# Kernel tuning notes

Hardware: AMD Instinct MI355X
Metric: run time of the kernel (lower is better)

Reference implementation:

```python
import jax, jax.numpy as jnp
import numpy as np

B, N, H, R = 128, 512, 256, 3
VIRTUAL_DECAY = 0.7


def _build_tree():
    # Deterministic random recursive tree: parent[i] ~ U[0, i)
    rng = np.random.default_rng(0)
    parent = np.zeros(N, np.int64)
    for i in range(1, N):
        parent[i] = rng.integers(0, i)
    depth = np.zeros(N, np.int64)
    for i in range(1, N):
        depth[i] = depth[parent[i]] + 1
    rel_edge = rng.integers(0, R, N)          # relation type of edge (parent -> i)
    virtual = rng.random(N) < 0.1
    children = [[] for _ in range(N)]
    for i in range(1, N):
        children[parent[i]].append(i)
    # Group internal nodes by depth (deepest first == valid post-order batching),
    # pad ragged child lists per level.
    levels = []
    for d in range(int(depth.max()), -1, -1):
        nodes = [n for n in range(N) if depth[n] == d and len(children[n]) > 0]
        if not nodes:
            continue
        cmax = max(len(children[n]) for n in nodes)
        M = len(nodes)
        cidx = np.zeros((M, cmax), np.int64)
        cmask = np.zeros((M, cmax), np.float32)
        crel = np.zeros((M, cmax), np.int64)
        cvirt = np.zeros((M, cmax), bool)
        for m, n in enumerate(nodes):
            ch = children[n]
            k = len(ch)
            cidx[m, :k] = ch
            cmask[m, :k] = 1.0
            crel[m, :k] = rel_edge[ch]
            cvirt[m, :k] = virtual[ch]
        levels.append((jnp.array(nodes), jnp.array(cidx), jnp.array(cmask),
                       jnp.array(crel), jnp.array(cvirt)))
    return levels

LEVELS = _build_tree()


def _forward(node_features, W_enc, b_enc, rel_emb, W_i, b_i, W_o, b_o, W_u, b_u,
             W_f, b_f, w_attn, b_attn):
    h = node_features @ W_enc + b_enc            # (B, N, H) node_encoder
    c = jnp.zeros_like(h)
    for node_ids, cidx, cmask, crel, cvirt in LEVELS:
        x = h[:, node_ids]                       # (B, M, H) input_vec (== encoded feats)
        ch_h = h[:, cidx]                        # (B, M, C, H)
        ch_c = c[:, cidx]
        # virtual-node decay + padding mask
        decay = jnp.where(cvirt, VIRTUAL_DECAY, 1.0).astype(h.dtype) * cmask  # (M, C)
        ch_h = ch_h * decay[None, :, :, None]
        ch_c = ch_c * decay[None, :, :, None]
        # relation-aware attention over children
        re = rel_emb[crel]                       # (M, C, H)
        scores = jnp.einsum('bmch,h->bmc', re[None] + ch_h, w_attn) + b_attn[0]
        scores = jnp.where(cmask[None] > 0, scores, -1e9)
        attw = jax.nn.softmax(scores, axis=-1)   # (B, M, C)
        h_sum = jnp.einsum('bmc,bmch->bmh', attw, ch_h)
        # per-relation forget transform (note: original applies NO sigmoid here)
        f = jnp.zeros_like(ch_h)
        for r in range(R):
            fr = jnp.einsum('bmch,hk->bmck', ch_h, W_f[r]) + b_f[r]
            f = f + fr * (crel == r).astype(h.dtype)[None, :, :, None]
        c_sum = jnp.sum(f * ch_c, axis=2)        # (B, M, H); padded ch_c is 0
        comb = jnp.concatenate([x, h_sum], axis=-1)  # (B, M, 2H)
        i_g = jax.nn.sigmoid(comb @ W_i + b_i)
        o_g = jax.nn.sigmoid(comb @ W_o + b_o)
        u_g = jnp.tanh(comb @ W_u + b_u)
        c_new = i_g * u_g + c_sum
        h_new = o_g * jnp.tanh(c_new)
        h = h.at[:, node_ids].set(h_new)
        c = c.at[:, node_ids].set(c_new)
    return h[:, 0]                               # pooling == 'root' (root = 0)


def setup_inputs() -> dict:
    key = jax.random.key(0)
    ks = jax.random.split(key, 8)
    s = 0.05
    f32 = jnp.float32
    return {
        'node_features': jax.random.normal(ks[0], (B, N, H), f32),
        'W_enc': jax.random.normal(ks[1], (H, H), f32) * s,
        'b_enc': jnp.full((H,), 0.1, f32),
        'rel_emb': jax.random.normal(ks[2], (R, H), f32) * s,
        'W_i': jax.random.normal(ks[3], (2 * H, H), f32) * s,
        'b_i': jnp.full((H,), 0.1, f32),
        'W_o': jax.random.normal(ks[4], (2 * H, H), f32) * s,
        'b_o': jnp.full((H,), 0.1, f32),
        'W_u': jax.random.normal(ks[5], (2 * H, H), f32) * s,
        'b_u': jnp.full((H,), 0.1, f32),
        'W_f': jax.random.normal(ks[6], (R, H, H), f32) * s,
        'b_f': jnp.full((R, H), 0.1, f32),
        'w_attn': jax.random.normal(ks[7], (H,), f32) * s,
        'b_attn': jnp.full((1,), 0.1, f32),
    }


def reference(node_features, W_enc, b_enc, rel_emb, W_i, b_i, W_o, b_o, W_u, b_u,
              W_f, b_f, w_attn, b_attn):
    return _forward(node_features, W_enc, b_enc, rel_emb, W_i, b_i, W_o, b_o,
                    W_u, b_u, W_f, b_f, w_attn, b_attn)
```

## Files before the change

### kernel.cpp

```cpp
#include <hip/hip_runtime.h>
#include <stdint.h>
#include <string.h>
#include <math.h>

#define NB 128
#define NN 512
#define NH 256
#define NR 3
#define TH_SPLIT 16

typedef __attribute__((ext_vector_type(8))) short bh8;
typedef __attribute__((ext_vector_type(4))) float f32x4;

struct Pcg {
  __uint128_t state, inc;
  bool has32; uint32_t buf32;
};

static const __uint128_t PCG_MULT =
    (((__uint128_t)2549297995355413924ULL) << 64) | 4865540595714422341ULL;

static inline uint64_t pcg_next64(Pcg& s) {
  s.state = s.state * PCG_MULT + s.inc;
  uint64_t hi = (uint64_t)(s.state >> 64), lo = (uint64_t)s.state;
  uint64_t x = hi ^ lo;
  unsigned rot = (unsigned)(s.state >> 122) & 63u;
  return (x >> rot) | (x << ((64u - rot) & 63u));
}
static inline uint32_t pcg_next32(Pcg& s) {
  if (s.has32) { s.has32 = false; return s.buf32; }
  uint64_t n = pcg_next64(s);
  s.has32 = true; s.buf32 = (uint32_t)(n >> 32);
  return (uint32_t)n;
}
static inline uint64_t pcg_bounded(Pcg& s, uint64_t high) {
  uint64_t rng = high - 1;
  if (rng == 0) return 0;
  uint32_t rng_excl = (uint32_t)rng + 1u;
  uint64_t m = (uint64_t)pcg_next32(s) * (uint64_t)rng_excl;
  uint32_t leftover = (uint32_t)m;
  if (leftover < rng_excl) {
    uint32_t threshold = (uint32_t)((0xFFFFFFFFu - (uint32_t)rng) % rng_excl);
// ... 19 lines not shown
  };
  for (int i = 0; i < 4; i++) pool[i] = hashmix(0u);
  for (int src = 0; src < 4; src++)
    for (int dst = 0; dst < 4; dst++)
      if (src != dst) pool[dst] = mix(pool[dst], hashmix(pool[src]));
  uint32_t gs[8]; uint32_t hb = 0x8b51f9ddu;
  for (int i = 0; i < 8; i++) {
    uint32_t dv = pool[i & 3];
    dv ^= hb; hb *= 0x58f38dedu; dv *= hb; dv ^= dv >> 16;
    gs[i] = dv;
  }
  uint64_t w0 = (uint64_t)gs[0] | ((uint64_t)gs[1] << 32);
  uint64_t w1 = (uint64_t)gs[2] | ((uint64_t)gs[3] << 32);
  uint64_t w2 = (uint64_t)gs[4] | ((uint64_t)gs[5] << 32);
  uint64_t w3 = (uint64_t)gs[6] | ((uint64_t)gs[7] << 32);
  __uint128_t initstate = (((__uint128_t)w0) << 64) | w1;
  __uint128_t initseq   = (((__uint128_t)w2) << 64) | w3;
  s.state = 0;
  s.inc = (initseq << 1) | 1;
  s.state = s.state * PCG_MULT + s.inc;
  s.state += initstate;
  s.state = s.state * PCG_MULT + s.inc;
  s.has32 = false; s.buf32 = 0;
}

struct TreeMeta {
  int nodes[512];
  int cstart[512];
  int ccount[512];
  int echild[512];
  int erel[512];
  float edecay[512];
  int cechild[512];
  int cerel[512];
  float cedec[512];
  int cens[513];
};
struct HostTree {
  TreeMeta meta;
  int n_levels;
  int level_off[520];
  int level_M[520];
};

static void build_tree_host(HostTree& T) {
  Pcg st; pcg_seed0(st);
  int parent[NN], depth[NN], rel[NN];
  unsigned char virt[NN];
  parent[0] = 0; depth[0] = 0;
  for (int i = 1; i < NN; i++) parent[i] = (int)pcg_bounded(st, (uint64_t)i);
  for (int i = 1; i < NN; i++) depth[i] = depth[parent[i]] + 1;
  for (int i = 0; i < NN; i++) rel[i] = (int)pcg_bounded(st, (uint64_t)NR);
  for (int i = 0; i < NN; i++) virt[i] = (pcg_double(st) < 0.1) ? 1 : 0;

  int childcnt[NN]; memset(childcnt, 0, sizeof(childcnt));
  for (int i = 1; i < NN; i++) childcnt[parent[i]]++;
  int maxd = 0;
  for (int i = 0; i < NN; i++) if (depth[i] > maxd) maxd = depth[i];

  int ni = 0, ne = 0, nec = 0;
  T.n_levels = 0;
  for (int d = maxd; d >= 0; d--) {
    int mstart = ni;
    for (int n = 0; n < NN; n++) {
      if (depth[n] == d && childcnt[n] > 0) {
        T.meta.nodes[ni] = n;
        T.meta.cstart[ni] = ne;
        T.meta.ccount[ni] = childcnt[n];
        T.meta.cens[ni] = nec;
        for (int i2 = 1; i2 < NN; i2++) {
          if (parent[i2] == n) {
            T.meta.echild[ne] = i2;
            T.meta.erel[ne] = rel[i2];
            T.meta.edecay[ne] = virt[i2] ? 0.7f : 1.0f;
            ne++;
            if (childcnt[i2] > 0) {
              T.meta.cechild[nec] = i2;
              T.meta.cerel[nec] = rel[i2];
              T.meta.cedec[nec] = virt[i2] ? 0.7f : 1.0f;
              nec++;
            }
          }
        }
        ni++;
      }
    }
    if (ni > mstart) {
      T.level_off[T.n_levels] = mstart;
      T.level_M[T.n_levels] = ni - mstart;
      T.n_levels++;
    }
  }
  T.meta.cens[ni] = nec;
}

__device__ __forceinline__ uint16_t f2bf(float f) {
  uint32_t u = __float_as_uint(f);
  return (uint16_t)((u + 0x7fffu + ((u >> 16) & 1u)) >> 16);
}
__device__ __forceinline__ float bf2f(uint16_t b) {
  return __uint_as_float(((uint32_t)b) << 16);
}
__device__ __forceinline__ float sigm(float x) {
  return 1.f / (1.f + expf(-x));
}

__device__ __forceinline__ void stage_bf16(uint16_t* __restrict__ sm,
    const uint16_t* __restrict__ src, int stride, int rows) {
  const int chunks = rows << 3;
  for (int cch = threadIdx.x; cch < chunks; cch += 256) {
// ... 84 lines not shown
  }
#pragma unroll
  for (int i = 0; i < 4; i++) {
#pragma unroll
    for (int j = 0; j < 4; j++) {
      const int col = bn + wc2 * 64 + j * 16 + (lane & 15);
      const float be = b_enc[col];
#pragma unroll
      for (int r = 0; r < 4; r++) {
        const int row = bm + wr * 64 + i * 16 + (lane >> 4) * 4 + r;
        const uint16_t hv = f2bf(acc[i][j][r] + be);
        h_bf[(size_t)row * NH + col] = hv;
        x_enc[(size_t)row * NH + col] = hv;
      }
    }
  }
}

__global__ __launch_bounds__(256) void k_sv0(const uint16_t* __restrict__ h_bf,
    const float* __restrict__ w_attn, float* __restrict__ svp) {
  const int idx = blockIdx.x * 256 + threadIdx.x;
  const int g = idx & 15;
  const size_t row = (size_t)(idx >> 4);
  const uint16_t* hp = h_bf + row * NH + g * 16;
  uint4 p0 = *(const uint4*)hp, p1 = *(const uint4*)(hp + 8);
  const uint16_t* e0 = (const uint16_t*)&p0;
  const uint16_t* e1 = (const uint16_t*)&p1;
  float s = 0.f;
#pragma unroll
  for (int u = 0; u < 8; u++) s = fmaf(bf2f(e0[u]), w_attn[g * 16 + u], s);
#pragma unroll
  for (int u = 0; u < 8; u++) s = fmaf(bf2f(e1[u]), w_attn[g * 16 + 8 + u], s);
  svp[idx] = s;
}

__global__ __launch_bounds__(256) void k_att(
    const uint16_t* __restrict__ h_bf, const float* __restrict__ svp,
    const float* __restrict__ rel_emb, const float* __restrict__ w_attn,
    const float* __restrict__ b_attn, uint16_t* __restrict__ comb,
    const TreeMeta* __restrict__ tm, int nb) {
  __shared__ float sc[64 * 65];
  __shared__ float sRE[3];
  __shared__ int chl[64]; __shared__ int rll[64]; __shared__ float dcl[64];
  const int mloc = blockIdx.x >> 1, b0 = (blockIdx.x & 1) * 64;
  const int gi = nb + mloc;
  const int cs = tm->cstart[gi], cc = tm->ccount[gi];
  const int tid = threadIdx.x, wid = tid >> 6, lane = tid & 63;

  if (tid < cc) {
    chl[tid] = tm->echild[cs + tid];
    rll[tid] = tm->erel[cs + tid];
    dcl[tid] = tm->edecay[cs + tid];
  }
  if (wid < 3) {
    float p = 0.f;
#pragma unroll
    for (int i = 0; i < 4; i++) p += rel_emb[wid * NH + lane + 64 * i] * w_attn[lane + 64 * i];
#pragma unroll
    for (int off = 32; off; off >>= 1) p += __shfl_down(p, off);
    if (lane == 0) sRE[wid] = p;
  }
  __syncthreads();

  const float ba = b_attn[0];
  if (tid < 64) {
    const float* svpb = svp + (size_t)(b0 + tid) * NN * 16;
    for (int e = 0; e < cc; e++) {
      const float4* p = (const float4*)(svpb + chl[e] * 16);
      float4 a = p[0], b2 = p[1], c2 = p[2], d2 = p[3];
      float s = ((a.x + a.y) + (a.z + a.w)) + ((b2.x + b2.y) + (b2.z + b2.w)) +
                ((c2.x + c2.y) + (c2.z + c2.w)) + ((d2.x + d2.y) + (d2.z + d2.w));
      sc[tid * 65 + e] = sRE[rll[e]] + dcl[e] * s + ba;
    }
    float mx = -1e30f;
    for (int e = 0; e < cc; e++) mx = fmaxf(mx, sc[tid * 65 + e]);
    float ss = 0.f;
    for (int e = 0; e < cc; e++) ss += expf(sc[tid * 65 + e] - mx);
    const float inv = 1.0f / ss;
    for (int e = 0; e < cc; e++) sc[tid * 65 + e] = expf(sc[tid * 65 + e] - mx) * inv * dcl[e];
  }
  __syncthreads();

  const int sb = tid >> 2, sq = tid & 3;
  float hs[64];
#pragma unroll
  for (int v = 0; v < 64; v++) hs[v] = 0.f;
  const uint16_t* hbase = h_bf + (size_t)(b0 + sb) * NN * NH + sq * 64;
  uint4 bufA[8], bufB[8];
  LDROW(bufA, chl[0]);
  int e = 0;
  for (; e + 2 <= cc; e += 2) {
    LDROW(bufB, chl[e + 1]);
    ACCROW(bufA, sc[sb * 65 + e]);
    if (e + 2 < cc) LDROW(bufA, chl[e + 2]);
    ACCROW(bufB, sc[sb * 65 + e + 1]);
  }
  if (e < cc) ACCROW(bufA, sc[sb * 65 + e]);
  uint16_t* cb = comb + ((size_t)(mloc * 128 + b0 + sb)) * 256 + sq * 64;
#pragma unroll
  for (int v = 0; v < 8; v++) {
    uint4 w;
    w.x = (uint32_t)f2bf(hs[8 * v + 0]) | ((uint32_t)f2bf(hs[8 * v + 1]) << 16);
    w.y = (uint32_t)f2bf(hs[8 * v + 2]) | ((uint32_t)f2bf(hs[8 * v + 3]) << 16);
    w.z = (uint32_t)f2bf(hs[8 * v + 4]) | ((uint32_t)f2bf(hs[8 * v + 5]) << 16);
    w.w = (uint32_t)f2bf(hs[8 * v + 6]) | ((uint32_t)f2bf(hs[8 * v + 7]) << 16);
    *(uint4*)(cb + v * 8) = w;
  }
}

__global__ __launch_bounds__(256) void k_gat(
    uint16_t* h_bf, float* c, float* __restrict__ svp,
    const uint16_t* __restrict__ x_enc, const uint16_t* __restrict__ comb,
    const uint16_t* __restrict__ WfT, const uint16_t* __restrict__ WgT,
    const float* __restrict__ b_f, const float* __restrict__ b_i,
    const float* __restrict__ b_o, const float* __restrict__ b_u,
    const float* __restrict__ w_attn, float* __restrict__ out,
    const TreeMeta* __restrict__ tm, int nb) {
  const int bx = blockIdx.x, mloc = bx >> 1, b0 = (bx & 1) * 64;
  const int cslice = blockIdx.y * 64;
  const int gi = nb + mloc;
  const int nd = tm->nodes[gi];
  const int ce0 = tm->cens[gi], nic = tm->cens[gi + 1] - ce0;
  const int tid = threadIdx.x, wid = tid >> 6, lane = tid & 63;
  const int lr2 = lane & 15, hi4 = (lane >> 4), lk = hi4 << 3;
  const int colw = cslice + wid * 16 + lr2;

  f32x4 csum[4] = {};
#pragma unroll 2
  for (int e = 0; e < nic; e++) {
    const int ch = tm->cechild[ce0 + e];
    const int rel = tm->cerel[ce0 + e];
    const float dec = tm->cedec[ce0 + e];
    const uint16_t* Wr = WfT + (size_t)rel * 65536 + (size_t)colw * 256;
    f32x4 facc[4] = {};
#pragma unroll
    for (int k0 = 0; k0 < 8; k0++) {
      const int kk = k0 * 32 + lk;
      bh8 af[4];
#pragma unroll
      for (int i = 0; i < 4; i++)
        af[i] = *(const bh8*)(h_bf + ((size_t)(b0 + i * 16 + lr2) * NN + ch) * NH + kk);
      const bh8 bq = *(const bh8*)(Wr + kk);
#pragma unroll
      for (int i = 0; i < 4; i++)
        facc[i] = __builtin_amdgcn_mfma_f32_16x16x32_bf16(af[i], bq, facc[i], 0, 0, 0);
    }
    const float bfv = b_f[rel * NH + colw];
#pragma unroll
    for (int i = 0; i < 4; i++) {
#pragma unroll
      for (int r = 0; r < 4; r++) {
        const int brow = b0 + i * 16 + hi4 * 4 + r;
        const float cch = c[((size_t)brow * NN + ch) * NH + colw];
        csum[i][r] += (dec * facc[i][r] + bfv) * (dec * cch);
      }
    }
  }

  f32x4 ga[3][4] = {};
#pragma unroll
  for (int k32 = 0; k32 < 16; k32++) {
    const int kk = k32 * 32 + lk;
    bh8 af[4], bq[3];
    if (k32 < 8) {
#pragma unroll
      for (int i = 0; i < 4; i++)
        af[i] = *(const bh8*)(x_enc + ((size_t)(b0 + i * 16 + lr2) * NN + nd) * NH + kk);
    } else {
#pragma unroll
      for (int i = 0; i < 4; i++)
        af[i] = *(const bh8*)(comb + ((size_t)(mloc * 128 + b0 + i * 16 + lr2)) * 256 + (kk - 256));
    }
#pragma unroll
    for (int g = 0; g < 3; g++)
      bq[g] = *(const bh8*)(WgT + ((size_t)g << 17) + (size_t)colw * 512 + kk);
#pragma unroll
    for (int g = 0; g < 3; g++)
#pragma unroll
      for (int i = 0; i < 4; i++)
        ga[g][i] = __builtin_amdgcn_mfma_f32_16x16x32_bf16(af[i], bq[g], ga[g][i], 0, 0, 0);
  }

  const float bi_ = b_i[colw], bo_ = b_o[colw], bu_ = b_u[colw];
  const float wac = w_attn[colw];
#pragma unroll
  for (int i = 0; i < 4; i++) {
#pragma unroll
    for (int r = 0; r < 4; r++) {
      const int brow = b0 + i * 16 + hi4 * 4 + r;
      const size_t idx = ((size_t)brow * NN + nd) * NH + colw;
      const float ig = sigm(ga[0][i][r] + bi_);
      const float og = sigm(ga[1][i][r] + bo_);
      const float ug = tanhf(ga[2][i][r] + bu_);
      const float cn = fmaf(ig, ug, csum[i][r]);
      c[idx] = cn;
      const float hn = og * tanhf(cn);
      h_bf[idx] = f2bf(hn);
      if (nd == 0) out[(size_t)brow * NH + colw] = hn;
      float pv = hn * wac;
      pv += __shfl_xor(pv, 1); pv += __shfl_xor(pv, 2);
      pv += __shfl_xor(pv, 4); pv += __shfl_xor(pv, 8);
      if (lr2 == 0) svp[((size_t)brow * NN + nd) * 16 + (cslice >> 4) + wid] = pv;
    }
  }
}

__global__ __launch_bounds__(256) void k_tiny(
    uint16_t* h_bf, float* c, float* __restrict__ svp,
    const uint16_t* __restrict__ x_enc,
    const uint16_t* __restrict__ WfT, const uint16_t* __restrict__ WgT,
    const float* __restrict__ b_f, const float* __restrict__ b_i,
    const float* __restrict__ b_o, const float* __restrict__ b_u,
    const float* __restrict__ rel_emb, const float* __restrict__ w_attn,
    const float* __restrict__ b_attn, float* __restrict__ out,
    const TreeMeta* __restrict__ tm, int nb) {
  __shared__ float sc[64 * 65];
  __shared__ float swa[256];
  __shared__ float sRE[3];
  __shared__ int chl[64]; __shared__ int rll[64]; __shared__ float dcl[64];
  __shared__ __align__(16) uint16_t hsum[4 * 4096];

  const int c0 = blockIdx.x * 16;
  const int mloc = blockIdx.y >> 1, b0 = (blockIdx.y & 1) * 64;
  const int gi = nb + mloc;
  const int nd = tm->nodes[gi], cs = tm->cstart[gi], cc = tm->ccount[gi];
  const int ce0 = tm->cens[gi], nic = tm->cens[gi + 1] - ce0;
  const int tid = threadIdx.x, wid = tid >> 6, lane = tid & 63;
  const int lb = lane & 15, lq = lane >> 4;
  const int colw = c0 + lb;
  const int wrow = b0 + wid * 16;

  if (tid < cc) {
    chl[tid] = tm->echild[cs + tid];
    rll[tid] = tm->erel[cs + tid];
    dcl[tid] = tm->edecay[cs + tid];
  }
  swa[tid] = w_attn[tid];
// ... 82 lines not shown
    const int kk = k32 * 32 + lq * 8;
    bh8 af;
    if (k32 < 8) {
      af = *(const bh8*)(x_enc + ((size_t)(wrow + lb) * NN + nd) * NH + kk);
    } else {
      const int kx = k32 - 8;
      af = fld(hsum + (kx >> 1) * 4096, wid * 16 + lb, (kx & 1) * 32 + lq * 8);
    }
#pragma unroll
    for (int g = 0; g < 3; g++) {
      const bh8 bq = *(const bh8*)(WgT + ((size_t)g << 17) + (size_t)colw * 512 + kk);
      ga[g] = __builtin_amdgcn_mfma_f32_16x16x32_bf16(af, bq, ga[g], 0, 0, 0);
    }
  }

  const float bi_ = b_i[colw], bo_ = b_o[colw], bu_ = b_u[colw];
  const float wac = swa[colw];
#pragma unroll
  for (int r = 0; r < 4; r++) {
    const int brow = wrow + lq * 4 + r;
    const size_t idx = ((size_t)brow * NN + nd) * NH + colw;
    const float ig = sigm(ga[0][r] + bi_);
    const float og = sigm(ga[1][r] + bo_);
    const float ug = tanhf(ga[2][r] + bu_);
    const float cn = fmaf(ig, ug, csum[r]);
    c[idx] = cn;
    const float hn = og * tanhf(cn);
    h_bf[idx] = f2bf(hn);
    if (nd == 0) out[(size_t)brow * NH + colw] = hn;
    float pv = hn * wac;
    pv += __shfl_xor(pv, 1); pv += __shfl_xor(pv, 2);
    pv += __shfl_xor(pv, 4); pv += __shfl_xor(pv, 8);
    if (lb == 0) svp[((size_t)brow * NN + nd) * 16 + (c0 >> 4)] = pv;
  }
}

extern "C" void kernel_launch(void* const* d_in, const int* in_sizes, int n_in,
                              void* d_out, int out_size, void* d_ws, size_t ws_size,
                              hipStream_t stream) {
  (void)in_sizes; (void)n_in; (void)out_size; (void)ws_size;
  const float* nf      = (const float*)d_in[0];
  const float* W_enc   = (const float*)d_in[1];
  const float* b_enc   = (const float*)d_in[2];
  const float* rel_emb = (const float*)d_in[3];
  const float* W_i     = (const float*)d_in[4];
  const float* b_i     = (const float*)d_in[5];
  const float* W_o     = (const float*)d_in[6];
  const float* b_o     = (const float*)d_in[7];
  const float* W_u     = (const float*)d_in[8];
  const float* b_u     = (const float*)d_in[9];
  const float* W_f     = (const float*)d_in[10];
  const float* b_f     = (const float*)d_in[11];
  const float* w_attn  = (const float*)d_in[12];
  const float* b_attn  = (const float*)d_in[13];
  float* out = (float*)d_out;

  static HostTree T;
  build_tree_host(T);

  char* ws = (char*)d_ws;
  const size_t OFF_HBF  = 32768;
  const size_t SZ_HBF   = (size_t)NB * NN * NH * 2;
  const size_t OFF_XE   = OFF_HBF + SZ_HBF;
  const size_t OFF_WET  = OFF_XE + SZ_HBF;
  const size_t OFF_WFT  = OFF_WET + 131072;
  const size_t OFF_WGT  = OFF_WFT + 393216;
  const size_t OFF_C    = OFF_WGT + 786432;
  const size_t SZ_C     = (size_t)NB * NN * NH * 4;
  const size_t OFF_SVP  = OFF_C + SZ_C;
  const size_t OFF_COMB = OFF_SVP + (size_t)NB * NN * 16 * 4;

  TreeMeta* dm = (TreeMeta*)ws;
  uint16_t* h_bf = (uint16_t*)(ws + OFF_HBF);
  uint16_t* x_enc = (uint16_t*)(ws + OFF_XE);
  uint16_t* WeT = (uint16_t*)(ws + OFF_WET);
  uint16_t* WfT = (uint16_t*)(ws + OFF_WFT);
  uint16_t* WgT = (uint16_t*)(ws + OFF_WGT);
  float* c = (float*)(ws + OFF_C);
  float* svp = (float*)(ws + OFF_SVP);
  uint16_t* comb = (uint16_t*)(ws + OFF_COMB);

  hipMemcpyAsync(dm, &T.meta, sizeof(TreeMeta), hipMemcpyHostToDevice, stream);

  k_prep<<<2560, 256, 0, stream>>>(W_enc, W_f, W_i, W_o, W_u, WeT, WfT, WgT);
  k_enc<<<dim3((NB * NN) / 128, 2), 256, 0, stream>>>(nf, WeT, b_enc, h_bf, x_enc);
  k_sv0<<<dim3((NB * NN * 16) / 256), 256, 0, stream>>>(h_bf, w_attn, svp);

  for (int l = 0; l < T.n_levels; l++) {
    const int Mfull = T.level_M[l];
    if (Mfull >= TH_SPLIT) {
      for (int c0 = 0; c0 < Mfull; c0 += 128) {
        const int Mc = (Mfull - c0) < 128 ? (Mfull - c0) : 128;
        const int nb = T.level_off[l] + c0;
        k_att<<<dim3(2 * Mc), 256, 0, stream>>>(h_bf, svp, rel_emb, w_attn,
            b_attn, comb, dm, nb);
        k_gat<<<dim3(2 * Mc, 4), 256, 0, stream>>>(h_bf, c, svp, x_enc, comb,
            WfT, WgT, b_f, b_i, b_o, b_u, w_attn, out, dm, nb);
      }
    } else {
      k_tiny<<<dim3(16, 2 * Mfull), 256, 0, stream>>>(h_bf, c, svp, x_enc,
          WfT, WgT, b_f, b_i, b_o, b_u, rel_emb, w_attn, b_attn, out, dm,
          T.level_off[l]);
    }
  }
}
```

Before: 703.6 us.

## Fuse attention into level kernel and split high-fanout nodes with atomic forget-gate blocks

Replaces the per-level k_att+k_gat pair with a fused k_lvl that computes the attention-weighted child sum into shared memory (swizzled bf16) and feeds it straight into the gate MFMAs, removing the comb round trip and one launch per level. For levels containing a node with many internal children, the forget-gate child GEMMs are spread over extra blocks in a combined k_ac kernel that accumulates f*c into the parent cell state via atomicAdd, followed by a separate k_gates kernel. The tiny-level threshold changes and c is now zeroed with a memset so atomics accumulate correctly. Fusing lowers launch and global-traffic cost but uses a large shared-memory footprint per block, and the atomic path makes float summation order nondeterministic.

New measurement: 622.7 us. -11.5%, faster.

```diff
diff --git a/kernel.cpp b/kernel.cpp
--- a/kernel.cpp
+++ b/kernel.cpp
@@ -7,7 +7,8 @@
 #define NN 512
 #define NH 256
 #define NR 3
-#define TH_SPLIT 16
+#define TH_TINY 24
+#define SPLIT_NIC 16
 
 typedef __attribute__((ext_vector_type(8))) short bh8;
 typedef __attribute__((ext_vector_type(4))) float f32x4;
@@ -93,6 +94,7 @@
   int erel[512];
   float edecay[512];
   int cechild[512];
+  int cepar[512];
   int cerel[512];
   float cedec[512];
   int cens[513];
@@ -137,6 +139,7 @@
             ne++;
             if (childcnt[i2] > 0) {
               T.meta.cechild[nec] = i2;
+              T.meta.cepar[nec] = n;
               T.meta.cerel[nec] = rel[i2];
               T.meta.cedec[nec] = virt[i2] ? 0.7f : 1.0f;
               nec++;
@@ -289,24 +292,36 @@
   svp[idx] = s;
 }
 
-__global__ __launch_bounds__(256) void k_att(
-    const uint16_t* __restrict__ h_bf, const float* __restrict__ svp,
+__global__ __launch_bounds__(256) void k_lvl(
+    uint16_t* h_bf, float* c, float* __restrict__ svp,
+    const uint16_t* __restrict__ x_enc,
+    const uint16_t* __restrict__ WfT, const uint16_t* __restrict__ WgT,
+    const float* __restrict__ b_f, const float* __restrict__ b_i,
+    const float* __restrict__ b_o, const float* __restrict__ b_u,
     const float* __restrict__ rel_emb, const float* __restrict__ w_attn,
-    const float* __restrict__ b_attn, uint16_t* __restrict__ comb,
+    const float* __restrict__ b_attn, float* __restrict__ out,
     const TreeMeta* __restrict__ tm, int nb) {
   __shared__ float sc[64 * 65];
+  __shared__ float swa[256];
   __shared__ float sRE[3];
   __shared__ int chl[64]; __shared__ int rll[64]; __shared__ float dcl[64];
-  const int mloc = blockIdx.x >> 1, b0 = (blockIdx.x & 1) * 64;
+  __shared__ __align__(16) uint16_t hsum[4 * 4096];
+
+  const int bx = blockIdx.x, mloc = bx >> 1, b0 = (bx & 1) * 64;
+  const int cslice = blockIdx.y * 64;
   const int gi = nb + mloc;
-  const int cs = tm->cstart[gi], cc = tm->ccount[gi];
+  const int nd = tm->nodes[gi], cs = tm->cstart[gi], cc = tm->ccount[gi];
+  const int ce0 = tm->cens[gi], nic = tm->cens[gi + 1] - ce0;
   const int tid = threadIdx.x, wid = tid >> 6, lane = tid & 63;
+  const int lr2 = lane & 15, hi4 = (lane >> 4), lk = hi4 << 3;
+  const int colw = cslice + wid * 16 + lr2;
 
   if (tid < cc) {
     chl[tid] = tm->echild[cs + tid];
     rll[tid] = tm->erel[cs + tid];
     dcl[tid] = tm->edecay[cs + tid];
   }
+  swa[tid] = w_attn[tid];
   if (wid < 3) {
     float p = 0.f;
 #pragma unroll
@@ -337,48 +352,29 @@
   __syncthreads();
 
   const int sb = tid >> 2, sq = tid & 3;
-  float hs[64];
-#pragma unroll
-  for (int v = 0; v < 64; v++) hs[v] = 0.f;
-  const uint16_t* hbase = h_bf + (size_t)(b0 + sb) * NN * NH + sq * 64;
-  uint4 bufA[8], bufB[8];
-  LDROW(bufA, chl[0]);
-  int e = 0;
-  for (; e + 2 <= cc; e += 2) {
-    LDROW(bufB, chl[e + 1]);
-    ACCROW(bufA, sc[sb * 65 + e]);
-    if (e + 2 < cc) LDROW(bufA, chl[e + 2]);
-    ACCROW(bufB, sc[sb * 65 + e + 1]);
-  }
-  if (e < cc) ACCROW(bufA, sc[sb * 65 + e]);
-  uint16_t* cb = comb + ((size_t)(mloc * 128 + b0 + sb)) * 256 + sq * 64;
-#pragma unroll
-  for (int v = 0; v < 8; v++) {
-    uint4 w;
-    w.x = (uint32_t)f2bf(hs[8 * v + 0]) | ((uint32_t)f2bf(hs[8 * v + 1]) << 16);
-    w.y = (uint32_t)f2bf(hs[8 * v + 2]) | ((uint32_t)f2bf(hs[8 * v + 3]) << 16);
-    w.z = (uint32_t)f2bf(hs[8 * v + 4]) | ((uint32_t)f2bf(hs[8 * v + 5]) << 16);
-    w.w = (uint32_t)f2bf(hs[8 * v + 6]) | ((uint32_t)f2bf(hs[8 * v + 7]) << 16);
-    *(uint4*)(cb + v * 8) = w;
-  }
-}
-
-__global__ __launch_bounds__(256) void k_gat(
-    uint16_t* h_bf, float* c, float* __restrict__ svp,
-    const uint16_t* __restrict__ x_enc, const uint16_t* __restrict__ comb,
-    const uint16_t* __restrict__ WfT, const uint16_t* __restrict__ WgT,
-    const float* __restrict__ b_f, const float* __restrict__ b_i,
-    const float* __restrict__ b_o, const float* __restrict__ b_u,
-    const float* __restrict__ w_attn, float* __restrict__ out,
-    const TreeMeta* __restrict__ tm, int nb) {
-  const int bx = blockIdx.x, mloc = bx >> 1, b0 = (bx & 1) * 64;
-  const int cslice = blockIdx.y * 64;
-  const int gi = nb + mloc;
-  const int nd = tm->nodes[gi];
-  const int ce0 = tm->cens[gi], nic = tm->cens[gi + 1] - ce0;
-  const int tid = threadIdx.x, wid = tid >> 6, lane = tid & 63;
-  const int lr2 = lane & 15, hi4 = (lane >> 4), lk = hi4 << 3;
-  const int colw = cslice + wid * 16 + lr2;
+  {
+    float hs[64];
+#pragma unroll
+    for (int v = 0; v < 64; v++) hs[v] = 0.f;
+    const uint16_t* hbase = h_bf + (size_t)(b0 + sb) * NN * NH + sq * 64;
+    uint4 bufA[8], bufB[8];
+    LDROW(bufA, chl[0]);
+    int e = 0;
+    for (; e + 2 <= cc; e += 2) {
+      LDROW(bufB, chl[e + 1]);
+      ACCROW(bufA, sc[sb * 65 + e]);
+      if (e + 2 < cc) LDROW(bufA, chl[e + 2]);
+      ACCROW(bufB, sc[sb * 65 + e + 1]);
+    }
+    if (e < cc) ACCROW(bufA, sc[sb * 65 + e]);
+    uint16_t* sub = hsum + sq * 4096;
+#pragma unroll
+    for (int v = 0; v < 32; v++) {
+      uint32_t pk = (uint32_t)f2bf(hs[2 * v]) | ((uint32_t)f2bf(hs[2 * v + 1]) << 16);
+      const int elem = ((sb << 6) + 2 * v) ^ ((sb & 7) << 3);
+      *(uint32_t*)(sub + elem) = pk;
+    }
+  }
 
   f32x4 csum[4] = {};
 #pragma unroll 2
@@ -411,6 +407,7 @@
       }
     }
   }
+  __syncthreads();
 
   f32x4 ga[3][4] = {};
 #pragma unroll
@@ -422,9 +419,10 @@
       for (int i = 0; i < 4; i++)
         af[i] = *(const bh8*)(x_enc + ((size_t)(b0 + i * 16 + lr2) * NN + nd) * NH + kk);
     } else {
-#pragma unroll
-      for (int i = 0; i < 4; i++)
-        af[i] = *(const bh8*)(comb + ((size_t)(mloc * 128 + b0 + i * 16 + lr2)) * 256 + (kk - 256));
+      const int kx = k32 - 8;
+#pragma unroll
+      for (int i = 0; i < 4; i++)
+        af[i] = fld(hsum + (kx >> 1) * 4096, i * 16 + lr2, (kx & 1) * 32 + lk);
     }
 #pragma unroll
     for (int g = 0; g < 3; g++)
@@ -437,7 +435,7 @@
   }
 
   const float bi_ = b_i[colw], bo_ = b_o[colw], bu_ = b_u[colw];
-  const float wac = w_attn[colw];
+  const float wac = swa[colw];
 #pragma unroll
   for (int i = 0; i < 4; i++) {
 #pragma unroll
@@ -606,6 +604,182 @@
     pv += __shfl_xor(pv, 1); pv += __shfl_xor(pv, 2);
     pv += __shfl_xor(pv, 4); pv += __shfl_xor(pv, 8);
     if (lb == 0) svp[((size_t)brow * NN + nd) * 16 + (c0 >> 4)] = pv;
+  }
+}
+
+__global__ __launch_bounds__(256) void k_ac(
+    const uint16_t* __restrict__ h_bf, float* c, const float* __restrict__ svp,
+    const uint16_t* __restrict__ WfT, const float* __restrict__ b_f,
+    const float* __restrict__ rel_emb, const float* __restrict__ w_attn,
+    const float* __restrict__ b_attn, uint16_t* __restrict__ comb,
+    const TreeMeta* __restrict__ tm, int nb, int M, int ce0) {
+  const int tid = threadIdx.x, wid = tid >> 6, lane = tid & 63;
+  const int bx = blockIdx.x;
+
+  if (bx >= 2 * M) {
+    const int e8 = bx - 2 * M;
+    const int ce = ce0 + (e8 >> 3);
+    const int sub = e8 & 7;
+    const int b0 = (sub >> 2) * 64, cslice = (sub & 3) * 64;
+    const int ch = tm->cechild[ce], par = tm->cepar[ce], rel = tm->cerel[ce];
+    const float dec = tm->cedec[ce];
+    const int lr2 = lane & 15, hi4 = lane >> 4, lk = hi4 << 3;
+    const int colw = cslice + wid * 16 + lr2;
+    const uint16_t* Wr = WfT + (size_t)rel * 65536 + (size_t)colw * 256;
+    f32x4 facc[4] = {};
+#pragma unroll
+    for (int k0 = 0; k0 < 8; k0++) {
+      const int kk = k0 * 32 + lk;
+      bh8 af[4];
+#pragma unroll
+      for (int i = 0; i < 4; i++)
+        af[i] = *(const bh8*)(h_bf + ((size_t)(b0 + i * 16 + lr2) * NN + ch) * NH + kk);
+      const bh8 bq = *(const bh8*)(Wr + kk);
+#pragma unroll
+      for (int i = 0; i < 4; i++)
+        facc[i] = __builtin_amdgcn_mfma_f32_16x16x32_bf16(af[i], bq, facc[i], 0, 0, 0);
+    }
+    const float bfv = b_f[rel * NH + colw];
+#pragma unroll
+    for (int i = 0; i < 4; i++) {
+#pragma unroll
+      for (int r = 0; r < 4; r++) {
+        const int brow = b0 + i * 16 + hi4 * 4 + r;
+        const float cch = c[((size_t)brow * NN + ch) * NH + colw];
+        atomicAdd(&c[((size_t)brow * NN + par) * NH + colw],
+                  (dec * facc[i][r] + bfv) * (dec * cch));
+      }
+    }
+  } else {
+    __shared__ float sc[64 * 65];
+    __shared__ float sRE[3];
+    __shared__ int chl[64]; __shared__ int rll[64]; __shared__ float dcl[64];
+    const int mloc = bx >> 1, b0 = (bx & 1) * 64;
+    const int gi = nb + mloc;
+    const int cs = tm->cstart[gi], cc = tm->ccount[gi];
+
+    if (tid < cc) {
+      chl[tid] = tm->echild[cs + tid];
+      rll[tid] = tm->erel[cs + tid];
+      dcl[tid] = tm->edecay[cs + tid];
+    }
+    if (wid < 3) {
+      float p = 0.f;
+#pragma unroll
+      for (int i = 0; i < 4; i++) p += rel_emb[wid * NH + lane + 64 * i] * w_attn[lane + 64 * i];
+#pragma unroll
+      for (int off = 32; off; off >>= 1) p += __shfl_down(p, off);
+      if (lane == 0) sRE[wid] = p;
+    }
+    __syncthreads();
+
+    const float ba = b_attn[0];
+    if (tid < 64) {
+      const float* svpb = svp + (size_t)(b0 + tid) * NN * 16;
+      for (int e = 0; e < cc; e++) {
+        const float4* p = (const float4*)(svpb + chl[e] * 16);
+        float4 a = p[0], b2 = p[1], c2 = p[2], d2 = p[3];
+        float s = ((a.x + a.y) + (a.z + a.w)) + ((b2.x + b2.y) + (b2.z + b2.w)) +
+                  ((c2.x + c2.y) + (c2.z + c2.w)) + ((d2.x + d2.y) + (d2.z + d2.w));
+        sc[tid * 65 + e] = sRE[rll[e]] + dcl[e] * s + ba;
+      }
+      float mx = -1e30f;
+      for (int e = 0; e < cc; e++) mx = fmaxf(mx, sc[tid * 65 + e]);
+      float ss = 0.f;
+      for (int e = 0; e < cc; e++) ss += expf(sc[tid * 65 + e] - mx);
+      const float inv = 1.0f / ss;
+      for (int e = 0; e < cc; e++) sc[tid * 65 + e] = expf(sc[tid * 65 + e] - mx) * inv * dcl[e];
+    }
+    __syncthreads();
+
+    const int sb = tid >> 2, sq = tid & 3;
+    float hs[64];
+#pragma unroll
+    for (int v = 0; v < 64; v++) hs[v] = 0.f;
+    const uint16_t* hbase = h_bf + (size_t)(b0 + sb) * NN * NH + sq * 64;
+    uint4 bufA[8], bufB[8];
+    LDROW(bufA, chl[0]);
+    int e = 0;
+    for (; e + 2 <= cc; e += 2) {
+      LDROW(bufB, chl[e + 1]);
+      ACCROW(bufA, sc[sb * 65 + e]);
+      if (e + 2 < cc) LDROW(bufA, chl[e + 2]);
+      ACCROW(bufB, sc[sb * 65 + e + 1]);
+    }
+    if (e < cc) ACCROW(bufA, sc[sb * 65 + e]);
+    uint16_t* cb = comb + ((size_t)(mloc * 128 + b0 + sb)) * 256 + sq * 64;
+#pragma unroll
+    for (int v = 0; v < 8; v++) {
+      uint4 w;
+      w.x = (uint32_t)f2bf(hs[8 * v + 0]) | ((uint32_t)f2bf(hs[8 * v + 1]) << 16);
+      w.y = (uint32_t)f2bf(hs[8 * v + 2]) | ((uint32_t)f2bf(hs[8 * v + 3]) << 16);
+      w.z = (uint32_t)f2bf(hs[8 * v + 4]) | ((uint32_t)f2bf(hs[8 * v + 5]) << 16);
+      w.w = (uint32_t)f2bf(hs[8 * v + 6]) | ((uint32_t)f2bf(hs[8 * v + 7]) << 16);
+      *(uint4*)(cb + v * 8) = w;
+    }
+  }
+}
+
+__global__ __launch_bounds__(256) void k_gates(
+    uint16_t* h_bf, float* c, float* __restrict__ svp,
+    const uint16_t* __restrict__ x_enc, const uint16_t* __restrict__ comb,
+    const uint16_t* __restrict__ WgT,
+    const float* __restrict__ b_i, const float* __restrict__ b_o,
+    const float* __restrict__ b_u, const float* __restrict__ w_attn,
+    float* __restrict__ out, const TreeMeta* __restrict__ tm, int nb) {
+  const int bx = blockIdx.x, mloc = bx >> 1, b0 = (bx & 1) * 64;
+  const int cslice = blockIdx.y * 64;
+  const int gi = nb + mloc;
+  const int nd = tm->nodes[gi];
+  const int tid = threadIdx.x, wid = tid >> 6, lane = tid & 63;
+  const int lr2 = lane & 15, hi4 = lane >> 4, lk = hi4 << 3;
+  const int colw = cslice + wid * 16 + lr2;
+
+  f32x4 ga[3][4] = {};
+#pragma unroll
+  for (int k32 = 0; k32 < 16; k32++) {
+    const int kk = k32 * 32 + lk;
+    bh8 af[4], bq[3];
+    if (k32 < 8) {
+#pragma unroll
+      for (int i = 0; i < 4; i++)
+        af[i] = *(const bh8*)(x_enc + ((size_t)(b0 + i * 16 + lr2) * NN + nd) * NH + kk);
+    } else {
+#pragma unroll
+      for (int i = 0; i < 4; i++)
+        af[i] = *(const bh8*)(comb + ((size_t)(mloc * 128 + b0 + i * 16 + lr2)) * 256 + (kk - 256));
+    }
+#pragma unroll
+    for (int g = 0; g < 3; g++)
+      bq[g] = *(const bh8*)(WgT + ((size_t)g << 17) + (size_t)colw * 512 + kk);
+#pragma unroll
+    for (int g = 0; g < 3; g++)
+#pragma unroll
+      for (int i = 0; i < 4; i++)
+        ga[g][i] = __builtin_amdgcn_mfma_f32_16x16x32_bf16(af[i], bq[g], ga[g][i], 0, 0, 0);
+  }
+
+  const float bi_ = b_i[colw], bo_ = b_o[colw], bu_ = b_u[colw];
+  const float wac = w_attn[colw];
+#pragma unroll
+  for (int i = 0; i < 4; i++) {
+#pragma unroll
+    for (int r = 0; r < 4; r++) {
+      const int brow = b0 + i * 16 + hi4 * 4 + r;
+      const size_t idx = ((size_t)brow * NN + nd) * NH + colw;
+      const float ig = sigm(ga[0][i][r] + bi_);
+      const float og = sigm(ga[1][i][r] + bo_);
+      const float ug = tanhf(ga[2][i][r] + bu_);
+      const float cn = fmaf(ig, ug, c[idx]);
+      c[idx] = cn;
+      const float hn = og * tanhf(cn);
+      h_bf[idx] = f2bf(hn);
+      if (nd == 0) out[(size_t)brow * NH + colw] = hn;
+      float pv = hn * wac;
+      pv += __shfl_xor(pv, 1); pv += __shfl_xor(pv, 2);
+      pv += __shfl_xor(pv, 4); pv += __shfl_xor(pv, 8);
+      if (lr2 == 0) svp[((size_t)brow * NN + nd) * 16 + (cslice >> 4) + wid] = pv;
+    }
   }
 }
 
@@ -655,6 +829,7 @@
   uint16_t* comb = (uint16_t*)(ws + OFF_COMB);
 
   hipMemcpyAsync(dm, &T.meta, sizeof(TreeMeta), hipMemcpyHostToDevice, stream);
+  hipMemsetAsync(c, 0, SZ_C, stream);
 
   k_prep<<<2560, 256, 0, stream>>>(W_enc, W_f, W_i, W_o, W_u, WeT, WfT, WgT);
   k_enc<<<dim3((NB * NN) / 128, 2), 256, 0, stream>>>(nf, WeT, b_enc, h_bf, x_enc);
@@ -662,19 +837,28 @@
 
   for (int l = 0; l < T.n_levels; l++) {
     const int Mfull = T.level_M[l];
-    if (Mfull >= TH_SPLIT) {
-      for (int c0 = 0; c0 < Mfull; c0 += 128) {
-        const int Mc = (Mfull - c0) < 128 ? (Mfull - c0) : 128;
-        const int nb = T.level_off[l] + c0;
-        k_att<<<dim3(2 * Mc), 256, 0, stream>>>(h_bf, svp, rel_emb, w_attn,
-            b_attn, comb, dm, nb);
-        k_gat<<<dim3(2 * Mc, 4), 256, 0, stream>>>(h_bf, c, svp, x_enc, comb,
-            WfT, WgT, b_f, b_i, b_o, b_u, w_attn, out, dm, nb);
+    for (int c0 = 0; c0 < Mfull; c0 += 128) {
+      const int Mc = (Mfull - c0) < 128 ? (Mfull - c0) : 128;
+      const int nb = T.level_off[l] + c0;
+      int maxnic = 0;
+      for (int m = 0; m < Mc; m++) {
+        const int nic = T.meta.cens[nb + m + 1] - T.meta.cens[nb + m];
+        if (nic > maxnic) maxnic = nic;
       }
-    } else {
-      k_tiny<<<dim3(16, 2 * Mfull), 256, 0, stream>>>(h_bf, c, svp, x_enc,
-          WfT, WgT, b_f, b_i, b_o, b_u, rel_emb, w_attn, b_attn, out, dm,
-          T.level_off[l]);
-    }
-  }
-}
+      if (maxnic >= SPLIT_NIC) {
+        const int ce0 = T.meta.cens[nb];
+        const int nCE = T.meta.cens[nb + Mc] - ce0;
+        k_ac<<<dim3(2 * Mc + 8 * nCE), 256, 0, stream>>>(h_bf, c, svp, WfT, b_f,
+            rel_emb, w_attn, b_attn, comb, dm, nb, Mc, ce0);
+        k_gates<<<dim3(2 * Mc, 4), 256, 0, stream>>>(h_bf, c, svp, x_enc, comb,
+            WgT, b_i, b_o, b_u, w_attn, out, dm, nb);
+      } else if (Mc >= TH_TINY) {
+        k_lvl<<<dim3(2 * Mc, 4), 256, 0, stream>>>(h_bf, c, svp, x_enc, WfT, WgT,
+            b_f, b_i, b_o, b_u, rel_emb, w_attn, b_attn, out, dm, nb);
+      } else {
+        k_tiny<<<dim3(16, 2 * Mc), 256, 0, stream>>>(h_bf, c, svp, x_enc,
+            WfT, WgT, b_f, b_i, b_o, b_u, rel_emb, w_attn, b_attn, out, dm, nb);
+      }
+    }
+  }
+}
```

## Split forget-gate work per child edge with atomics and merge into attention kernel

Applied to the files above, without the earlier changes.

Moves the per-child forget-gate GEMM out of the gate kernel into separate blocks, one set per internal-child edge. These blocks are launched in the same grid as the attention blocks and atomically accumulate into the parent's cell state, so the serial per-node loop over children becomes edge-level parallelism. The gate kernel now reads the pre-accumulated c. To support this, c is zeroed with a memset up front and the tiny-kernel threshold changes. This risks atomic contention on nodes with many internal children, adds a full memset of c, and makes summation order nondeterministic.

Result: faster. 628.3 us (-10.7%).

```diff
diff --git a/kernel.cpp b/kernel.cpp
--- a/kernel.cpp
+++ b/kernel.cpp
@@ -7,7 +7,8 @@
 #define NN 512
 #define NH 256
 #define NR 3
-#define TH_SPLIT 16
+#define TH_TINY 24
+#define SPLIT_M 24
 
 typedef __attribute__((ext_vector_type(8))) short bh8;
 typedef __attribute__((ext_vector_type(4))) float f32x4;
@@ -93,6 +94,7 @@
   int erel[512];
   float edecay[512];
   int cechild[512];
+  int cepar[512];
   int cerel[512];
   float cedec[512];
   int cens[513];
@@ -137,6 +139,7 @@
             ne++;
             if (childcnt[i2] > 0) {
               T.meta.cechild[nec] = i2;
+              T.meta.cepar[nec] = n;
               T.meta.cerel[nec] = rel[i2];
               T.meta.cedec[nec] = virt[i2] ? 0.7f : 1.0f;
               nec++;
@@ -287,177 +290,6 @@
 #pragma unroll
   for (int u = 0; u < 8; u++) s = fmaf(bf2f(e1[u]), w_attn[g * 16 + 8 + u], s);
   svp[idx] = s;
-}
-
-__global__ __launch_bounds__(256) void k_att(
-    const uint16_t* __restrict__ h_bf, const float* __restrict__ svp,
-    const float* __restrict__ rel_emb, const float* __restrict__ w_attn,
-    const float* __restrict__ b_attn, uint16_t* __restrict__ comb,
-    const TreeMeta* __restrict__ tm, int nb) {
-  __shared__ float sc[64 * 65];
-  __shared__ float sRE[3];
-  __shared__ int chl[64]; __shared__ int rll[64]; __shared__ float dcl[64];
-  const int mloc = blockIdx.x >> 1, b0 = (blockIdx.x & 1) * 64;
-  const int gi = nb + mloc;
-  const int cs = tm->cstart[gi], cc = tm->ccount[gi];
-  const int tid = threadIdx.x, wid = tid >> 6, lane = tid & 63;
-
-  if (tid < cc) {
-    chl[tid] = tm->echild[cs + tid];
-    rll[tid] = tm->erel[cs + tid];
-    dcl[tid] = tm->edecay[cs + tid];
-  }
-  if (wid < 3) {
-    float p = 0.f;
-#pragma unroll
-    for (int i = 0; i < 4; i++) p += rel_emb[wid * NH + lane + 64 * i] * w_attn[lane + 64 * i];
-#pragma unroll
-    for (int off = 32; off; off >>= 1) p += __shfl_down(p, off);
-    if (lane == 0) sRE[wid] = p;
-  }
-  __syncthreads();
-
-  const float ba = b_attn[0];
-  if (tid < 64) {
-    const float* svpb = svp + (size_t)(b0 + tid) * NN * 16;
-    for (int e = 0; e < cc; e++) {
-      const float4* p = (const float4*)(svpb + chl[e] * 16);
-      float4 a = p[0], b2 = p[1], c2 = p[2], d2 = p[3];
-      float s = ((a.x + a.y) + (a.z + a.w)) + ((b2.x + b2.y) + (b2.z + b2.w)) +
-                ((c2.x + c2.y) + (c2.z + c2.w)) + ((d2.x + d2.y) + (d2.z + d2.w));
-      sc[tid * 65 + e] = sRE[rll[e]] + dcl[e] * s + ba;
-    }
-    float mx = -1e30f;
-    for (int e = 0; e < cc; e++) mx = fmaxf(mx, sc[tid * 65 + e]);
-    float ss = 0.f;
-    for (int e = 0; e < cc; e++) ss += expf(sc[tid * 65 + e] - mx);
-    const float inv = 1.0f / ss;
-    for (int e = 0; e < cc; e++) sc[tid * 65 + e] = expf(sc[tid * 65 + e] - mx) * inv * dcl[e];
-  }
-  __syncthreads();
-
-  const int sb = tid >> 2, sq = tid & 3;
-  float hs[64];
-#pragma unroll
-  for (int v = 0; v < 64; v++) hs[v] = 0.f;
-  const uint16_t* hbase = h_bf + (size_t)(b0 + sb) * NN * NH + sq * 64;
-  uint4 bufA[8], bufB[8];
-  LDROW(bufA, chl[0]);
-  int e = 0;
-  for (; e + 2 <= cc; e += 2) {
-    LDROW(bufB, chl[e + 1]);
-    ACCROW(bufA, sc[sb * 65 + e]);
-    if (e + 2 < cc) LDROW(bufA, chl[e + 2]);
-    ACCROW(bufB, sc[sb * 65 + e + 1]);
-  }
-  if (e < cc) ACCROW(bufA, sc[sb * 65 + e]);
-  uint16_t* cb = comb + ((size_t)(mloc * 128 + b0 + sb)) * 256 + sq * 64;
-#pragma unroll
-  for (int v = 0; v < 8; v++) {
-    uint4 w;
-    w.x = (uint32_t)f2bf(hs[8 * v + 0]) | ((uint32_t)f2bf(hs[8 * v + 1]) << 16);
-    w.y = (uint32_t)f2bf(hs[8 * v + 2]) | ((uint32_t)f2bf(hs[8 * v + 3]) << 16);
-    w.z = (uint32_t)f2bf(hs[8 * v + 4]) | ((uint32_t)f2bf(hs[8 * v + 5]) << 16);
-    w.w = (uint32_t)f2bf(hs[8 * v + 6]) | ((uint32_t)f2bf(hs[8 * v + 7]) << 16);
-    *(uint4*)(cb + v * 8) = w;
-  }
-}
-
-__global__ __launch_bounds__(256) void k_gat(
-    uint16_t* h_bf, float* c, float* __restrict__ svp,
-    const uint16_t* __restrict__ x_enc, const uint16_t* __restrict__ comb,
-    const uint16_t* __restrict__ WfT, const uint16_t* __restrict__ WgT,
-    const float* __restrict__ b_f, const float* __restrict__ b_i,
-    const float* __restrict__ b_o, const float* __restrict__ b_u,
-    const float* __restrict__ w_attn, float* __restrict__ out,
-    const TreeMeta* __restrict__ tm, int nb) {
-  const int bx = blockIdx.x, mloc = bx >> 1, b0 = (bx & 1) * 64;
-  const int cslice = blockIdx.y * 64;
-  const int gi = nb + mloc;
-  const int nd = tm->nodes[gi];
-  const int ce0 = tm->cens[gi], nic = tm->cens[gi + 1] - ce0;
-  const int tid = threadIdx.x, wid = tid >> 6, lane = tid & 63;
-  const int lr2 = lane & 15, hi4 = (lane >> 4), lk = hi4 << 3;
-  const int colw = cslice + wid * 16 + lr2;
-
-  f32x4 csum[4] = {};
-#pragma unroll 2
-  for (int e = 0; e < nic; e++) {
-    const int ch = tm->cechild[ce0 + e];
-    const int rel = tm->cerel[ce0 + e];
-    const float dec = tm->cedec[ce0 + e];
-    const uint16_t* Wr = WfT + (size_t)rel * 65536 + (size_t)colw * 256;
-    f32x4 facc[4] = {};
-#pragma unroll
-    for (int k0 = 0; k0 < 8; k0++) {
-      const int kk = k0 * 32 + lk;
-      bh8 af[4];
-#pragma unroll
-      for (int i = 0; i < 4; i++)
-        af[i] = *(const bh8*)(h_bf + ((size_t)(b0 + i * 16 + lr2) * NN + ch) * NH + kk);
-      const bh8 bq = *(const bh8*)(Wr + kk);
-#pragma unroll
-      for (int i = 0; i < 4; i++)
-        facc[i] = __builtin_amdgcn_mfma_f32_16x16x32_bf16(af[i], bq, facc[i], 0, 0, 0);
-    }
-    const float bfv = b_f[rel * NH + colw];
-#pragma unroll
-    for (int i = 0; i < 4; i++) {
-#pragma unroll
-      for (int r = 0; r < 4; r++) {
-        const int brow = b0 + i * 16 + hi4 * 4 + r;
-        const float cch = c[((size_t)brow * NN + ch) * NH + colw];
-        csum[i][r] += (dec * facc[i][r] + bfv) * (dec * cch);
-      }
-    }
-  }
-
-  f32x4 ga[3][4] = {};
-#pragma unroll
-  for (int k32 = 0; k32 < 16; k32++) {
-    const int kk = k32 * 32 + lk;
-    bh8 af[4], bq[3];
-    if (k32 < 8) {
-#pragma unroll
-      for (int i = 0; i < 4; i++)
-        af[i] = *(const bh8*)(x_enc + ((size_t)(b0 + i * 16 + lr2) * NN + nd) * NH + kk);
-    } else {
-#pragma unroll
-      for (int i = 0; i < 4; i++)
-        af[i] = *(const bh8*)(comb + ((size_t)(mloc * 128 + b0 + i * 16 + lr2)) * 256 + (kk - 256));
-    }
-#pragma unroll
-    for (int g = 0; g < 3; g++)
-      bq[g] = *(const bh8*)(WgT + ((size_t)g << 17) + (size_t)colw * 512 + kk);
-#pragma unroll
-    for (int g = 0; g < 3; g++)
-#pragma unroll
-      for (int i = 0; i < 4; i++)
-        ga[g][i] = __builtin_amdgcn_mfma_f32_16x16x32_bf16(af[i], bq[g], ga[g][i], 0, 0, 0);
-  }
-
-  const float bi_ = b_i[colw], bo_ = b_o[colw], bu_ = b_u[colw];
-  const float wac = w_attn[colw];
-#pragma unroll
-  for (int i = 0; i < 4; i++) {
-#pragma unroll
-    for (int r = 0; r < 4; r++) {
-      const int brow = b0 + i * 16 + hi4 * 4 + r;
-      const size_t idx = ((size_t)brow * NN + nd) * NH + colw;
-      const float ig = sigm(ga[0][i][r] + bi_);
-      const float og = sigm(ga[1][i][r] + bo_);
-      const float ug = tanhf(ga[2][i][r] + bu_);
-      const float cn = fmaf(ig, ug, csum[i][r]);
-      c[idx] = cn;
-      const float hn = og * tanhf(cn);
-      h_bf[idx] = f2bf(hn);
-      if (nd == 0) out[(size_t)brow * NH + colw] = hn;
-      float pv = hn * wac;
-      pv += __shfl_xor(pv, 1); pv += __shfl_xor(pv, 2);
-      pv += __shfl_xor(pv, 4); pv += __shfl_xor(pv, 8);
-      if (lr2 == 0) svp[((size_t)brow * NN + nd) * 16 + (cslice >> 4) + wid] = pv;
-    }
-  }
 }
 
 __global__ __launch_bounds__(256) void k_tiny(
@@ -606,6 +438,182 @@
     pv += __shfl_xor(pv, 1); pv += __shfl_xor(pv, 2);
     pv += __shfl_xor(pv, 4); pv += __shfl_xor(pv, 8);
     if (lb == 0) svp[((size_t)brow * NN + nd) * 16 + (c0 >> 4)] = pv;
+  }
+}
+
+__global__ __launch_bounds__(256) void k_ac(
+    const uint16_t* __restrict__ h_bf, float* c, const float* __restrict__ svp,
+    const uint16_t* __restrict__ WfT, const float* __restrict__ b_f,
+    const float* __restrict__ rel_emb, const float* __restrict__ w_attn,
+    const float* __restrict__ b_attn, uint16_t* __restrict__ comb,
+    const TreeMeta* __restrict__ tm, int nb, int M, int ce0) {
+  const int tid = threadIdx.x, wid = tid >> 6, lane = tid & 63;
+  const int bx = blockIdx.x;
+
+  if (bx >= 2 * M) {
+    const int e8 = bx - 2 * M;
+    const int ce = ce0 + (e8 >> 3);
+    const int sub = e8 & 7;
+    const int b0 = (sub >> 2) * 64, cslice = (sub & 3) * 64;
+    const int ch = tm->cechild[ce], par = tm->cepar[ce], rel = tm->cerel[ce];
+    const float dec = tm->cedec[ce];
+    const int lr2 = lane & 15, hi4 = lane >> 4, lk = hi4 << 3;
+    const int colw = cslice + wid * 16 + lr2;
+    const uint16_t* Wr = WfT + (size_t)rel * 65536 + (size_t)colw * 256;
+    f32x4 facc[4] = {};
+#pragma unroll
+    for (int k0 = 0; k0 < 8; k0++) {
+      const int kk = k0 * 32 + lk;
+      bh8 af[4];
+#pragma unroll
+      for (int i = 0; i < 4; i++)
+        af[i] = *(const bh8*)(h_bf + ((size_t)(b0 + i * 16 + lr2) * NN + ch) * NH + kk);
+      const bh8 bq = *(const bh8*)(Wr + kk);
+#pragma unroll
+      for (int i = 0; i < 4; i++)
+        facc[i] = __builtin_amdgcn_mfma_f32_16x16x32_bf16(af[i], bq, facc[i], 0, 0, 0);
+    }
+    const float bfv = b_f[rel * NH + colw];
+#pragma unroll
+    for (int i = 0; i < 4; i++) {
+#pragma unroll
+      for (int r = 0; r < 4; r++) {
+        const int brow = b0 + i * 16 + hi4 * 4 + r;
+        const float cch = c[((size_t)brow * NN + ch) * NH + colw];
+        atomicAdd(&c[((size_t)brow * NN + par) * NH + colw],
+                  (dec * facc[i][r] + bfv) * (dec * cch));
+      }
+    }
+  } else {
+    __shared__ float sc[64 * 65];
+    __shared__ float sRE[3];
+    __shared__ int chl[64]; __shared__ int rll[64]; __shared__ float dcl[64];
+    const int mloc = bx >> 1, b0 = (bx & 1) * 64;
+    const int gi = nb + mloc;
+    const int cs = tm->cstart[gi], cc = tm->ccount[gi];
+
+    if (tid < cc) {
+      chl[tid] = tm->echild[cs + tid];
+      rll[tid] = tm->erel[cs + tid];
+      dcl[tid] = tm->edecay[cs + tid];
+    }
+    if (wid < 3) {
+      float p = 0.f;
+#pragma unroll
+      for (int i = 0; i < 4; i++) p += rel_emb[wid * NH + lane + 64 * i] * w_attn[lane + 64 * i];
+#pragma unroll
+      for (int off = 32; off; off >>= 1) p += __shfl_down(p, off);
+      if (lane == 0) sRE[wid] = p;
+    }
+    __syncthreads();
+
+    const float ba = b_attn[0];
+    if (tid < 64) {
+      const float* svpb = svp + (size_t)(b0 + tid) * NN * 16;
+      for (int e = 0; e < cc; e++) {
+        const float4* p = (const float4*)(svpb + chl[e] * 16);
+        float4 a = p[0], b2 = p[1], c2 = p[2], d2 = p[3];
+        float s = ((a.x + a.y) + (a.z + a.w)) + ((b2.x + b2.y) + (b2.z + b2.w)) +
+                  ((c2.x + c2.y) + (c2.z + c2.w)) + ((d2.x + d2.y) + (d2.z + d2.w));
+        sc[tid * 65 + e] = sRE[rll[e]] + dcl[e] * s + ba;
+      }
+      float mx = -1e30f;
+      for (int e = 0; e < cc; e++) mx = fmaxf(mx, sc[tid * 65 + e]);
+      float ss = 0.f;
+      for (int e = 0; e < cc; e++) ss += expf(sc[tid * 65 + e] - mx);
+      const float inv = 1.0f / ss;
+      for (int e = 0; e < cc; e++) sc[tid * 65 + e] = expf(sc[tid * 65 + e] - mx) * inv * dcl[e];
+    }
+    __syncthreads();
+
+    const int sb = tid >> 2, sq = tid & 3;
+    float hs[64];
+#pragma unroll
+    for (int v = 0; v < 64; v++) hs[v] = 0.f;
+    const uint16_t* hbase = h_bf + (size_t)(b0 + sb) * NN * NH + sq * 64;
+    uint4 bufA[8], bufB[8];
+    LDROW(bufA, chl[0]);
+    int e = 0;
+    for (; e + 2 <= cc; e += 2) {
+      LDROW(bufB, chl[e + 1]);
+      ACCROW(bufA, sc[sb * 65 + e]);
+      if (e + 2 < cc) LDROW(bufA, chl[e + 2]);
+      ACCROW(bufB, sc[sb * 65 + e + 1]);
+    }
+    if (e < cc) ACCROW(bufA, sc[sb * 65 + e]);
+    uint16_t* cb = comb + ((size_t)(mloc * 128 + b0 + sb)) * 256 + sq * 64;
+#pragma unroll
+    for (int v = 0; v < 8; v++) {
+      uint4 w;
+      w.x = (uint32_t)f2bf(hs[8 * v + 0]) | ((uint32_t)f2bf(hs[8 * v + 1]) << 16);
+      w.y = (uint32_t)f2bf(hs[8 * v + 2]) | ((uint32_t)f2bf(hs[8 * v + 3]) << 16);
+      w.z = (uint32_t)f2bf(hs[8 * v + 4]) | ((uint32_t)f2bf(hs[8 * v + 5]) << 16);
+      w.w = (uint32_t)f2bf(hs[8 * v + 6]) | ((uint32_t)f2bf(hs[8 * v + 7]) << 16);
+      *(uint4*)(cb + v * 8) = w;
+    }
+  }
+}
+
+__global__ __launch_bounds__(256) void k_gates(
+    uint16_t* h_bf, float* c, float* __restrict__ svp,
+    const uint16_t* __restrict__ x_enc, const uint16_t* __restrict__ comb,
+    const uint16_t* __restrict__ WgT,
+    const float* __restrict__ b_i, const float* __restrict__ b_o,
+    const float* __restrict__ b_u, const float* __restrict__ w_attn,
+    float* __restrict__ out, const TreeMeta* __restrict__ tm, int nb) {
+  const int bx = blockIdx.x, mloc = bx >> 1, b0 = (bx & 1) * 64;
+  const int cslice = blockIdx.y * 64;
+  const int gi = nb + mloc;
+  const int nd = tm->nodes[gi];
+  const int tid = threadIdx.x, wid = tid >> 6, lane = tid & 63;
+  const int lr2 = lane & 15, hi4 = lane >> 4, lk = hi4 << 3;
+  const int colw = cslice + wid * 16 + lr2;
+
+  f32x4 ga[3][4] = {};
+#pragma unroll
+  for (int k32 = 0; k32 < 16; k32++) {
+    const int kk = k32 * 32 + lk;
+    bh8 af[4], bq[3];
+    if (k32 < 8) {
+#pragma unroll
+      for (int i = 0; i < 4; i++)
+        af[i] = *(const bh8*)(x_enc + ((size_t)(b0 + i * 16 + lr2) * NN + nd) * NH + kk);
+    } else {
+#pragma unroll
+      for (int i = 0; i < 4; i++)
+        af[i] = *(const bh8*)(comb + ((size_t)(mloc * 128 + b0 + i * 16 + lr2)) * 256 + (kk - 256));
+    }
+#pragma unroll
+    for (int g = 0; g < 3; g++)
+      bq[g] = *(const bh8*)(WgT + ((size_t)g << 17) + (size_t)colw * 512 + kk);
+#pragma unroll
+    for (int g = 0; g < 3; g++)
+#pragma unroll
+      for (int i = 0; i < 4; i++)
+        ga[g][i] = __builtin_amdgcn_mfma_f32_16x16x32_bf16(af[i], bq[g], ga[g][i], 0, 0, 0);
+  }
+
+  const float bi_ = b_i[colw], bo_ = b_o[colw], bu_ = b_u[colw];
+  const float wac = w_attn[colw];
+#pragma unroll
+  for (int i = 0; i < 4; i++) {
+#pragma unroll
+    for (int r = 0; r < 4; r++) {
+      const int brow = b0 + i * 16 + hi4 * 4 + r;
+      const size_t idx = ((size_t)brow * NN + nd) * NH + colw;
+      const float ig = sigm(ga[0][i][r] + bi_);
+      const float og = sigm(ga[1][i][r] + bo_);
+      const float ug = tanhf(ga[2][i][r] + bu_);
+      const float cn = fmaf(ig, ug, c[idx]);
+      c[idx] = cn;
+      const float hn = og * tanhf(cn);
+      h_bf[idx] = f2bf(hn);
+      if (nd == 0) out[(size_t)brow * NH + colw] = hn;
+      float pv = hn * wac;
+      pv += __shfl_xor(pv, 1); pv += __shfl_xor(pv, 2);
+      pv += __shfl_xor(pv, 4); pv += __shfl_xor(pv, 8);
+      if (lr2 == 0) svp[((size_t)brow * NN + nd) * 16 + (cslice >> 4) + wid] = pv;
+    }
   }
 }
 
@@ -655,6 +663,7 @@
   uint16_t* comb = (uint16_t*)(ws + OFF_COMB);
 
   hipMemcpyAsync(dm, &T.meta, sizeof(TreeMeta), hipMemcpyHostToDevice, stream);
+  hipMemsetAsync(c, 0, SZ_C, stream);
 
   k_prep<<<2560, 256, 0, stream>>>(W_enc, W_f, W_i, W_o, W_u, WeT, WfT, WgT);
   k_enc<<<dim3((NB * NN) / 128, 2), 256, 0, stream>>>(nf, WeT, b_enc, h_bf, x_enc);
@@ -662,19 +671,20 @@
 
   for (int l = 0; l < T.n_levels; l++) {
     const int Mfull = T.level_M[l];
-    if (Mfull >= TH_SPLIT) {
-      for (int c0 = 0; c0 < Mfull; c0 += 128) {
-        const int Mc = (Mfull - c0) < 128 ? (Mfull - c0) : 128;
-        const int nb = T.level_off[l] + c0;
-        k_att<<<dim3(2 * Mc), 256, 0, stream>>>(h_bf, svp, rel_emb, w_attn,
-            b_attn, comb, dm, nb);
-        k_gat<<<dim3(2 * Mc, 4), 256, 0, stream>>>(h_bf, c, svp, x_enc, comb,
-            WfT, WgT, b_f, b_i, b_o, b_u, w_attn, out, dm, nb);
+    for (int c0 = 0; c0 < Mfull; c0 += 128) {
+      const int Mc = (Mfull - c0) < 128 ? (Mfull - c0) : 128;
+      const int nb = T.level_off[l] + c0;
+      if (Mc >= SPLIT_M) {
+        const int ce0 = T.meta.cens[nb];
+        const int nCE = T.meta.cens[nb + Mc] - ce0;
+        k_ac<<<dim3(2 * Mc + 8 * nCE), 256, 0, stream>>>(h_bf, c, svp, WfT, b_f,
+            rel_emb, w_attn, b_attn, comb, dm, nb, Mc, ce0);
+        k_gates<<<dim3(2 * Mc, 4), 256, 0, stream>>>(h_bf, c, svp, x_enc, comb,
+            WgT, b_i, b_o, b_u, w_attn, out, dm, nb);
+      } else {
+        k_tiny<<<dim3(16, 2 * Mc), 256, 0, stream>>>(h_bf, c, svp, x_enc,
+            WfT, WgT, b_f, b_i, b_o, b_u, rel_emb, w_attn, b_attn, out, dm, nb);
       }
-    } else {
-      k_tiny<<<dim3(16, 2 * Mfull), 256, 0, stream>>>(h_bf, c, svp, x_enc,
-          WfT, WgT, b_f, b_i, b_o, b_u, rel_emb, w_attn, b_attn, out, dm,
-          T.level_off[l]);
-    }
-  }
-}
+    }
+  }
+}
```
